# Performance work log

Hardware: AMD Instinct MI355X
Metric: run time of the kernel (lower is better)

The kernel has to match this reference:

```python
import jax, jax.numpy as jnp
import numpy as np


def setup_inputs() -> dict:
    key = jax.random.key(0)
    k1, k2, k3 = jax.random.split(key, 3)
    B, L, D = 4, 4096, 1024
    inputs = jax.random.normal(k1, (B, L, D), dtype=jnp.float32)
    # nn.Linear(2D, 2D): weight [out=2D, in=2D], bias [2D]
    W_gate = jax.random.normal(k2, (2 * D, 2 * D), dtype=jnp.float32) * (1.0 / np.sqrt(2 * D))
    b_gate = jax.random.normal(k3, (2 * D,), dtype=jnp.float32) * 0.01
    return {"inputs": inputs, "W_gate": W_gate, "b_gate": b_gate}


def reference(inputs, W_gate, b_gate):
    B, L, D = inputs.shape
    # Cumulative average: tril(ones)/arange mask matmul == prefix-mean (linear time)
    denom = jnp.arange(1, L + 1, dtype=inputs.dtype)[None, :, None]  # [1, L, 1]
    average_outputs = jnp.cumsum(inputs, axis=1) / denom  # [B, L, D]
    # Gating linear on concat(inputs, avg): y = x @ W^T + b
    cat = jnp.concatenate([inputs, average_outputs], axis=-1)  # [B, L, 2D]
    gating = jnp.einsum('bld,ed->ble', cat, W_gate) + b_gate  # [B, L, 2D]
    input_gate, forget_gate = jnp.split(gating, 2, axis=-1)
    gating_outputs = (jax.nn.sigmoid(input_gate) * inputs
                      + jax.nn.sigmoid(forget_gate) * average_outputs)
    return gating_outputs, average_outputs
```

## Files before the change

### kernel.cpp

```cpp
#include <hip/hip_runtime.h>

#define B_   4
#define L_   4096
#define D_   1024
#define ROWS (B_ * L_)
#define K2   (2 * D_)
#define BLD  (ROWS * D_)
#define CH   128
#define NC   32

typedef __attribute__((ext_vector_type(8))) short s8v;
typedef __attribute__((ext_vector_type(4))) float f4v;

__device__ __forceinline__ unsigned short f2bf(float f) {
    unsigned int u = __float_as_uint(f);
    u += 0x7FFFu + ((u >> 16) & 1u);
    return (unsigned short)(u >> 16);
}

__device__ __forceinline__ float sigmoidf_(float v) {
    return 1.0f / (1.0f + __expf(-v));
}

__device__ __forceinline__ void llds16(const void* g, void* l) {
    __builtin_amdgcn_global_load_lds(
        (const __attribute__((address_space(1))) unsigned int*)(g),
        (__attribute__((address_space(3))) unsigned int*)(l),
        16, 0, 0);
}


__global__ void partial_sums(const float* __restrict__ x, float* __restrict__ part) {
    int bid  = blockIdx.x;
    int dblk = bid & 3;
    int c    = (bid >> 2) & 31;
    int b    = bid >> 7;
    int d    = dblk * 256 + threadIdx.x;
    const float* p = x + ((size_t)(b * L_ + c * CH) * D_ + d);
    float s = 0.f;
#pragma unroll 8
    for (int i = 0; i < CH; ++i) s += p[(size_t)i * D_];
    part[(b * NC + c) * D_ + d] = s;
}

__global__ void scan_chunks(float* __restrict__ part) {
    int idx = blockIdx.x * 256 + threadIdx.x;
    int b = idx >> 10, d = idx & 1023;
    float run = 0.f;
#pragma unroll
    for (int c = 0; c < NC; ++c) {
        int o = (b * NC + c) * D_ + d;
        float t = part[o];
        part[o] = run;
        run += t;
    }
}

__global__ void apply_scan(const float* __restrict__ x, const float* __restrict__ part,
                           float* __restrict__ avg_out, unsigned short* __restrict__ Abf) {
    int bid  = blockIdx.x;
    int dblk = bid & 3;
    int c    = (bid >> 2) & 31;
    int b    = bid >> 7;
    int d    = dblk * 256 + threadIdx.x;
    size_t row0 = (size_t)b * L_ + (size_t)c * CH;
    const float* p = x + (row0 * D_ + d);
    float s = part[(b * NC + c) * D_ + d];
    for (int i = 0; i < CH; ++i) {
        size_t row = row0 + i;
        float xi = p[(size_t)i * D_];
        s += xi;
        float av = s / (float)(c * CH + i + 1);
        avg_out[row * D_ + d]      = av;
        Abf[row * K2 + d]          = f2bf(xi);
        Abf[row * K2 + D_ + d]     = f2bf(av);
    }
}

__global__ void conv_w(const float4* __restrict__ W, ushort4* __restrict__ Wbf) {
    int t = blockIdx.x * 256 + threadIdx.x;
    float4 v = W[t];
    ushort4 o;
    o.x = f2bf(v.x); o.y = f2bf(v.y); o.z = f2bf(v.z); o.w = f2bf(v.w);
    Wbf[t] = o;
}

__global__ __launch_bounds__(256, 2) void gemm_gated(
        const unsigned short* __restrict__ Abf, const unsigned short* __restrict__ Wbf,
        const float* __restrict__ x, const float* __restrict__ avg,
        const float* __restrict__ bg, float* __restrict__ out) {
    __shared__ __attribute__((aligned(16))) unsigned short sA [128 * 32];
    __shared__ __attribute__((aligned(16))) unsigned short sB0[128 * 32];
    __shared__ __attribute__((aligned(16))) unsigned short sB1[128 * 32];

    const int t    = threadIdx.x;
    const int w    = t >> 6;
    const int lane = t & 63;
    const int bid  = blockIdx.x;
    const int tileN = bid & 7, tileM = bid >> 3;
    const int row0 = tileM * 128, col0 = tileN * 128;
    const int wm = w >> 1, wn = w & 1;
    const int quad = lane >> 4, lcol = lane & 15;

    f4v acc0[4][4], acc1[4][4];
#pragma unroll
    for (int i = 0; i < 4; ++i)
#pragma unroll
        for (int j = 0; j < 4; ++j)
#pragma unroll
            for (int r = 0; r < 4; ++r) { acc0[i][j][r] = 0.f; acc1[i][j][r] = 0.f; }

    const int c0 = t, c1 = 256 + t;
    const unsigned short* gA0 = Abf + ((size_t)(row0 + (c0 >> 2)) * K2 + (c0 & 3) * 8);
    const unsigned short* gA1 = Abf + ((size_t)(row0 + (c1 >> 2)) * K2 + (c1 & 3) * 8);
    const unsigned short* gB0a = Wbf + ((size_t)(col0 + (c0 >> 2)) * K2 + (c0 & 3) * 8);
    const unsigned short* gB0b = Wbf + ((size_t)(col0 + (c1 >> 2)) * K2 + (c1 & 3) * 8);
    const unsigned short* gB1a = Wbf + ((size_t)(col0 + 1024 + (c0 >> 2)) * K2 + (c0 & 3) * 8);
    const unsigned short* gB1b = Wbf + ((size_t)(col0 + 1024 + (c1 >> 2)) * K2 + (c1 & 3) * 8);
    unsigned short* lA0  = &sA [w * 512];
    unsigned short* lA1  = &sA [2048 + w * 512];
    unsigned short* lB0a = &sB0[w * 512];
    unsigned short* lB0b = &sB0[2048 + w * 512];
    unsigned short* lB1a = &sB1[w * 512];
    unsigned short* lB1b = &sB1[2048 + w * 512];

    for (int k0 = 0; k0 < K2; k0 += 32) {
        __syncthreads();
        llds16(gA0  + k0, lA0);
        llds16(gA1  + k0, lA1);
        llds16(gB0a + k0, lB0a);
        llds16(gB0b + k0, lB0b);
        llds16(gB1a + k0, lB1a);
        llds16(gB1b + k0, lB1b);
        __syncthreads();

        s8v af[4], bf0[4], bf1[4];
#pragma unroll
        for (int i = 0; i < 4; ++i)
            af[i] = *(const s8v*)&sA[(wm * 64 + i * 16 + lcol) * 32 + quad * 8];
#pragma unroll
        for (int j = 0; j < 4; ++j) {
            bf0[j] = *(const s8v*)&sB0[(wn * 64 + j * 16 + lcol) * 32 + quad * 8];
            bf1[j] = *(const s8v*)&sB1[(wn * 64 + j * 16 + lcol) * 32 + quad * 8];
        }
#pragma unroll
        for (int i = 0; i < 4; ++i)
#pragma unroll
            for (int j = 0; j < 4; ++j) {
                acc0[i][j] = __builtin_amdgcn_mfma_f32_16x16x32_bf16(af[i], bf0[j], acc0[i][j], 0, 0, 0);
                acc1[i][j] = __builtin_amdgcn_mfma_f32_16x16x32_bf16(af[i], bf1[j], acc1[i][j], 0, 0, 0);
            }
    }

    float b1v[4], b2v[4];
#pragma unroll
    for (int j = 0; j < 4; ++j) {
        int cc = col0 + wn * 64 + j * 16 + lcol;
        b1v[j] = bg[cc];
        b2v[j] = bg[1024 + cc];
    }
#pragma unroll
    for (int i = 0; i < 4; ++i) {
#pragma unroll
        for (int j = 0; j < 4; ++j) {
            int rr = row0 + wm * 64 + i * 16 + quad * 4;
            int cc = col0 + wn * 64 + j * 16 + lcol;
#pragma unroll
            for (int r = 0; r < 4; ++r) {
                size_t off = (size_t)(rr + r) * D_ + cc;
                float gi = sigmoidf_(acc0[i][j][r] + b1v[j]);
                float gf = sigmoidf_(acc1[i][j][r] + b2v[j]);
                out[off] = gi * x[off] + gf * avg[off];
            }
        }
    }
}

extern "C" void kernel_launch(void* const* d_in, const int* in_sizes, int n_in,
                              void* d_out, int out_size, void* d_ws, size_t ws_size,
                              hipStream_t stream) {
    const float* x  = (const float*)d_in[0];
    const float* W  = (const float*)d_in[1];
    const float* bg = (const float*)d_in[2];
    float* out = (float*)d_out;
    float* avg = out + (size_t)BLD;

    char* ws = (char*)d_ws;
    unsigned short* Abf = (unsigned short*)(ws);
    unsigned short* Wbf = (unsigned short*)(ws + (size_t)67108864);
    float*          prt = (float*)(ws + (size_t)75497472);

    conv_w<<<dim3(4096), dim3(256), 0, stream>>>((const float4*)W, (ushort4*)Wbf);
    partial_sums<<<dim3(512), dim3(256), 0, stream>>>(x, prt);
    scan_chunks<<<dim3(16), dim3(256), 0, stream>>>(prt);
    apply_scan<<<dim3(512), dim3(256), 0, stream>>>(x, prt, avg, Abf);
    gemm_gated<<<dim3(1024), dim3(256), 0, stream>>>(Abf, Wbf, x, avg, bg, out);
}
```

Measured before the change: 393.5 us.

## Fuse scan, chunk-prefix and weight conversion into one single-pass lookback kernel

```diff
diff --git a/kernel.cpp b/kernel.cpp
--- a/kernel.cpp
+++ b/kernel.cpp
@@ -8,6 +8,7 @@
 #define BLD  (ROWS * D_)
 #define CH   128
 #define NC   32
+#define MAGIC 0x5CA7F00Du
 
 typedef __attribute__((ext_vector_type(8))) short s8v;
 typedef __attribute__((ext_vector_type(4))) float f4v;
@@ -29,60 +30,67 @@
         16, 0, 0);
 }
 
-
-__global__ void partial_sums(const float* __restrict__ x, float* __restrict__ part) {
-    int bid  = blockIdx.x;
-    int dblk = bid & 3;
-    int c    = (bid >> 2) & 31;
-    int b    = bid >> 7;
-    int d    = dblk * 256 + threadIdx.x;
-    const float* p = x + ((size_t)(b * L_ + c * CH) * D_ + d);
-    float s = 0.f;
-#pragma unroll 8
-    for (int i = 0; i < CH; ++i) s += p[(size_t)i * D_];
-    part[(b * NC + c) * D_ + d] = s;
-}
-
-__global__ void scan_chunks(float* __restrict__ part) {
-    int idx = blockIdx.x * 256 + threadIdx.x;
-    int b = idx >> 10, d = idx & 1023;
-    float run = 0.f;
-#pragma unroll
-    for (int c = 0; c < NC; ++c) {
-        int o = (b * NC + c) * D_ + d;
-        float t = part[o];
-        part[o] = run;
-        run += t;
-    }
-}
-
-__global__ void apply_scan(const float* __restrict__ x, const float* __restrict__ part,
-                           float* __restrict__ avg_out, unsigned short* __restrict__ Abf) {
-    int bid  = blockIdx.x;
-    int dblk = bid & 3;
-    int c    = (bid >> 2) & 31;
-    int b    = bid >> 7;
-    int d    = dblk * 256 + threadIdx.x;
-    size_t row0 = (size_t)b * L_ + (size_t)c * CH;
-    const float* p = x + (row0 * D_ + d);
-    float s = part[(b * NC + c) * D_ + d];
-    for (int i = 0; i < CH; ++i) {
-        size_t row = row0 + i;
-        float xi = p[(size_t)i * D_];
-        s += xi;
-        float av = s / (float)(c * CH + i + 1);
-        avg_out[row * D_ + d]      = av;
-        Abf[row * K2 + d]          = f2bf(xi);
-        Abf[row * K2 + D_ + d]     = f2bf(av);
-    }
-}
-
-__global__ void conv_w(const float4* __restrict__ W, ushort4* __restrict__ Wbf) {
-    int t = blockIdx.x * 256 + threadIdx.x;
-    float4 v = W[t];
-    ushort4 o;
-    o.x = f2bf(v.x); o.y = f2bf(v.y); o.z = f2bf(v.z); o.w = f2bf(v.w);
-    Wbf[t] = o;
+__global__ __launch_bounds__(256) void scan_conv(
+        const float* __restrict__ x, const float* __restrict__ W,
+        float* __restrict__ avg_out, unsigned int* __restrict__ Apk,
+        ushort4* __restrict__ Wbf, float* __restrict__ part,
+        unsigned int* __restrict__ flag) {
+    const int bid = blockIdx.x;
+    const int t   = threadIdx.x;
+
+    if (bid < 512) {
+        const int dblk = bid & 3;
+        const int c    = (bid >> 2) & 31;
+        const int b    = bid >> 7;
+        const int d    = dblk * 256 + t;
+        const size_t row0 = (size_t)b * L_ + (size_t)c * CH;
+        const float* p = x + row0 * D_ + d;
+
+        float xv[CH];
+        float s = 0.f;
+#pragma unroll
+        for (int i = 0; i < CH; ++i) { xv[i] = p[(size_t)i * D_]; s += xv[i]; }
+
+        part[bid * 256 + t] = s;
+        __threadfence();
+        __syncthreads();
+        if (t == 0)
+            __hip_atomic_store(&flag[bid], MAGIC, __ATOMIC_RELEASE, __HIP_MEMORY_SCOPE_AGENT);
+
+        float prefix = 0.f;
+        for (int cp = c - 1; cp >= 0; --cp) {
+            const int pb = bid - 4 * (c - cp);
+            while (__hip_atomic_load(&flag[pb], __ATOMIC_ACQUIRE, __HIP_MEMORY_SCOPE_AGENT) != MAGIC)
+                __builtin_amdgcn_s_sleep(1);
+            prefix += part[pb * 256 + t];
+        }
+
+        __shared__ float inv[CH];
+        if (t < CH) inv[t] = 1.0f / (float)(c * CH + t + 1);
+        __syncthreads();
+        float run = prefix;
+#pragma unroll
+        for (int i = 0; i < CH; ++i) {
+            const size_t row = row0 + i;
+            run += xv[i];
+            const float av = run * inv[i];
+            avg_out[row * D_ + d] = av;
+            const unsigned int packed =
+                (unsigned int)f2bf(xv[i]) | ((unsigned int)f2bf(av) << 16);
+            Apk[row * (K2 / 2) + d] = packed;
+        }
+    } else {
+        const int idx = (bid - 512) * 256 + t;
+        const int e   = idx >> 8;
+        const int k4  = idx & 255;
+        const float4 v1 = ((const float4*)W)[(size_t)e * 512 + k4];
+        const float4 v2 = ((const float4*)W)[(size_t)e * 512 + 256 + k4];
+        ushort4 o0, o1;
+        o0.x = f2bf(v1.x); o0.y = f2bf(v2.x); o0.z = f2bf(v1.y); o0.w = f2bf(v2.y);
+        o1.x = f2bf(v1.z); o1.y = f2bf(v2.z); o1.z = f2bf(v1.w); o1.w = f2bf(v2.w);
+        Wbf[(size_t)e * 512 + 2 * k4]     = o0;
+        Wbf[(size_t)e * 512 + 2 * k4 + 1] = o1;
+    }
 }
 
 __global__ __launch_bounds__(256, 2) void gemm_gated(
@@ -189,10 +197,9 @@
     unsigned short* Abf = (unsigned short*)(ws);
     unsigned short* Wbf = (unsigned short*)(ws + (size_t)67108864);
     float*          prt = (float*)(ws + (size_t)75497472);
-
-    conv_w<<<dim3(4096), dim3(256), 0, stream>>>((const float4*)W, (ushort4*)Wbf);
-    partial_sums<<<dim3(512), dim3(256), 0, stream>>>(x, prt);
-    scan_chunks<<<dim3(16), dim3(256), 0, stream>>>(prt);
-    apply_scan<<<dim3(512), dim3(256), 0, stream>>>(x, prt, avg, Abf);
+    unsigned int*   flg = (unsigned int*)(ws + (size_t)76021760);
+
+    scan_conv<<<dim3(2560), dim3(256), 0, stream>>>(
+        x, W, avg, (unsigned int*)Abf, (ushort4*)Wbf, prt, flg);
     gemm_gated<<<dim3(1024), dim3(256), 0, stream>>>(Abf, Wbf, x, avg, bg, out);
 }
```

Result: slower. 678.6 us (+72.5%).
